# Kernel tuning notes

Measured on AMD Instinct MI355X. Metric: run time of the kernel, lower is better.

The kernel has to match this reference:

```python
import jax, jax.numpy as jnp
import numpy as np

B, S, D, H, MEL = 64, 512, 512, 8, 80
HD = D // H  # head dim


def _lstm_cell(x, h, c, w_ih, w_hh, b_ih, b_hh):
    # torch gate order: i, f, g, o
    gates = x @ w_ih.T + h @ w_hh.T + b_ih + b_hh
    i, f, g, o = jnp.split(gates, 4, axis=-1)
    c = jax.nn.sigmoid(f) * c + jax.nn.sigmoid(i) * jnp.tanh(g)
    h = jax.nn.sigmoid(o) * jnp.tanh(c)
    return h, c


def setup_inputs() -> dict:
    key = jax.random.key(0)
    ks = jax.random.split(key, 24)
    s = 0.05
    inp = {"encoder_output": jax.random.normal(ks[0], (B, S, D), jnp.float32)}
    # MultiheadAttention params (torch layout: in_proj [3D, D])
    inp["attn_in_w"] = jax.random.normal(ks[1], (3 * D, D), jnp.float32) * s
    inp["attn_in_b"] = jax.random.normal(ks[2], (3 * D,), jnp.float32) * s
    inp["attn_out_w"] = jax.random.normal(ks[3], (D, D), jnp.float32) * s
    inp["attn_out_b"] = jax.random.normal(ks[4], (D,), jnp.float32) * s
    # LSTM1 (2 layers)
    names = [("l1_w_ih0", (4 * D, D)), ("l1_w_hh0", (4 * D, D)), ("l1_b_ih0", (4 * D,)), ("l1_b_hh0", (4 * D,)),
             ("l1_w_ih1", (4 * D, D)), ("l1_w_hh1", (4 * D, D)), ("l1_b_ih1", (4 * D,)), ("l1_b_hh1", (4 * D,)),
             ("l2_w_ih", (4 * D, D)), ("l2_w_hh", (4 * D, D)), ("l2_b_ih", (4 * D,)), ("l2_b_hh", (4 * D,)),
             ("proj_w", (MEL, D)), ("proj_b", (MEL,))]
    for i, (n, shp) in enumerate(names):
        inp[n] = jax.random.normal(ks[5 + i], shp, jnp.float32) * s
    return inp


def reference(encoder_output, attn_in_w, attn_in_b, attn_out_w, attn_out_b,
              l1_w_ih0, l1_w_hh0, l1_b_ih0, l1_b_hh0,
              l1_w_ih1, l1_w_hh1, l1_b_ih1, l1_b_hh1,
              l2_w_ih, l2_w_hh, l2_b_ih, l2_b_hh, proj_w, proj_b):
    b, s, d = encoder_output.shape
    max_len = s * 5
    wq, wk, wv = jnp.split(attn_in_w, 3, axis=0)
    bq, bk, bv = jnp.split(attn_in_b, 3, axis=0)
    # Precompute K, V over encoder output: [B, S, H, HD]
    K = (encoder_output @ wk.T + bk).reshape(b, s, H, HD)
    V = (encoder_output @ wv.T + bv).reshape(b, s, H, HD)
    scale = 1.0 / np.sqrt(HD)

    def attend(x):  # x: [B, D] single-token query
        q = ((x @ wq.T + bq) * scale).reshape(b, H, HD)
        scores = jnp.einsum('bhd,bshd->bhs', q, K)
        w = jax.nn.softmax(scores, axis=-1)
        ctx = jnp.einsum('bhs,bshd->bhd', w, V).reshape(b, d)
        return ctx @ attn_out_w.T + attn_out_b

    zeros = jnp.zeros((b, d), encoder_output.dtype)
    carry0 = (zeros, zeros, zeros, zeros, zeros, zeros, zeros)

    def step(carry, _):
        h10, c10, h11, c11, h2, c2, dec_in = carry
        h10, c10 = _lstm_cell(dec_in, h10, c10, l1_w_ih0, l1_w_hh0, l1_b_ih0, l1_b_hh0)
        h11, c11 = _lstm_cell(h10, h11, c11, l1_w_ih1, l1_w_hh1, l1_b_ih1, l1_b_hh1)
        attn_out = attend(h11)
        h2, c2 = _lstm_cell(attn_out, h2, c2, l2_w_ih, l2_w_hh, l2_b_ih, l2_b_hh)
        out = h2 @ proj_w.T + proj_b  # [B, MEL]
        return (h10, c10, h11, c11, h2, c2, h2), out

    _, ys = jax.lax.scan(step, carry0, None, length=max_len)
    return jnp.transpose(ys, (1, 0, 2))  # [B, max_len, MEL]
```

## Files before the change

### kernel.cpp

```cpp
#include <hip/hip_runtime.h>
#include <hip/hip_bf16.h>
#include <hip/hip_fp8.h>

#define DEV_INLINE __device__ __forceinline__

typedef __attribute__((ext_vector_type(8))) short bf16x8;
typedef __attribute__((ext_vector_type(4))) float f32x4;
typedef unsigned long long ull;

constexpr int Bc = 64, Sc = 512, Dc = 512, Hc = 8, HDc = 64, MELc = 80, Tc = 2560;
constexpr int OUTSTRIDE = Tc * MELc;

constexpr size_t SZ_KP8 = 64ull * 8 * 512 * 64;
constexpr size_t SZ_VP8 = 64ull * 8 * 512 * 64;
constexpr size_t SZ_PL  = 128ull * 2048 * 16;
constexpr size_t OFF_KP8 = 0;
constexpr size_t OFF_VP8 = OFF_KP8 + SZ_KP8;
constexpr size_t OFF_PL0 = OFF_VP8 + SZ_VP8;
constexpr size_t OFF_PL1 = OFF_PL0 + SZ_PL;
constexpr size_t OFF_PL2 = OFF_PL1 + SZ_PL;
constexpr size_t OFF_PWQ = OFF_PL2 + SZ_PL;
constexpr size_t OFF_PP  = OFF_PWQ + 524288;
constexpr size_t OFF_BL0 = OFF_PP + 81920;
constexpr size_t OFF_BL1 = OFF_BL0 + 8192;
constexpr size_t OFF_BL2 = OFF_BL1 + 8192;
constexpr size_t OFF_B2E = OFF_BL2 + 8192;
constexpr size_t OFF_W2E = OFF_B2E + 8192;
constexpr size_t OFF_WOT = OFF_W2E + 2097152;
constexpr size_t OFF_ACT = OFF_WOT + 1048576;
constexpr size_t OFF_CTR = OFF_ACT + 524288;

constexpr unsigned LDS_WL0  = 0;
constexpr unsigned LDS_WL1  = 32768;
constexpr unsigned LDS_WL2  = 65536;
constexpr unsigned LDS_WPJ  = 98304;
constexpr unsigned LDS_PRED = 114688;
constexpr unsigned LDS_QLS  = 118784;
constexpr unsigned LDS_SCO  = 123136;
constexpr unsigned LDS_RED  = 127232;
constexpr unsigned LDS_CST  = 135424;
constexpr unsigned LDS_ST64 = 136960;
constexpr unsigned LDS_MISC = 137216;
constexpr unsigned DYN_LDS  = 137344;

DEV_INLINE unsigned* ctr_ptr(unsigned* base, int idx) { return base + idx * 32; }

DEV_INLINE float bf2f(short s) { return __uint_as_float(((unsigned)(unsigned short)s) << 16); }
DEV_INLINE short f2bf(float f) { union { __hip_bfloat16 h; short s; } u; u.h = __float2bfloat16(f); return u.s; }
DEV_INLINE float sig_f(float x) { return 1.0f / (1.0f + __expf(-x)); }
DEV_INLINE float tanh_f(float x) {
  float ax = fabsf(x);
  float e = __expf(fminf(2.0f * ax, 80.0f));
  float r = 1.0f - 2.0f / (e + 1.0f);
  return copysignf(r, x);
}
DEV_INLINE bf16x8 cvt8(const float* p) {
  bf16x8 r;
#pragma unroll
  for (int i = 0; i < 8; ++i) r[i] = f2bf(p[i]);
  return r;
}
DEV_INLINE float fp8tof(unsigned v) {
  __hip_fp8_e4m3 t; t.__x = (__hip_fp8_storage_t)v; return (float)t;
}

DEV_INLINE ull ld_dev_u64(const void* p) {
  return __hip_atomic_load((const ull*)p, __ATOMIC_RELAXED, __HIP_MEMORY_SCOPE_AGENT);
}
DEV_INLINE void st_dev_u64(void* p, ull v) {
  __hip_atomic_store((ull*)p, v, __ATOMIC_RELAXED, __HIP_MEMORY_SCOPE_AGENT);
}
DEV_INLINE bf16x8 ld_frag(const __hip_bfloat16* p) {
  union { bf16x8 v; ull u[2]; } r;
  r.u[0] = ld_dev_u64(p);
  r.u[1] = ld_dev_u64((const char*)p + 8);
  return r.v;
}

__global__ __launch_bounds__(256) void gemm_setup(const float* __restrict__ A,
                                                  const float* __restrict__ Bt,
                                                  const float* __restrict__ bias,
                                                  __hip_bfloat16* __restrict__ dst,
                                                  unsigned char* __restrict__ dst8,
                                                  int mode) {
  int tid = threadIdx.x, lane = tid & 63, wv = tid >> 6;
  int m0 = blockIdx.y * 64 + wv * 16;
  int nb = blockIdx.x * 64;
  int mrow = m0 + (lane & 15);
  int kb = (lane >> 4) * 8;
  f32x4 acc0 = {0,0,0,0}, acc1 = {0,0,0,0}, acc2 = {0,0,0,0}, acc3 = {0,0,0,0};
  const float* arow = A + (size_t)mrow * 512 + kb;
  const float* b0r = Bt + (size_t)(nb + 0 * 16 + (lane & 15)) * 512 + kb;
  const float* b1r = Bt + (size_t)(nb + 1 * 16 + (lane & 15)) * 512 + kb;
  const float* b2r = Bt + (size_t)(nb + 2 * 16 + (lane & 15)) * 512 + kb;
  const float* b3r = Bt + (size_t)(nb + 3 * 16 + (lane & 15)) * 512 + kb;
  for (int kk = 0; kk < 16; ++kk) {
    bf16x8 af = cvt8(arow + kk * 32);
    acc0 = __builtin_amdgcn_mfma_f32_16x16x32_bf16(af, cvt8(b0r + kk * 32), acc0, 0, 0, 0);
    acc1 = __builtin_amdgcn_mfma_f32_16x16x32_bf16(af, cvt8(b1r + kk * 32), acc1, 0, 0, 0);
    acc2 = __builtin_amdgcn_mfma_f32_16x16x32_bf16(af, cvt8(b2r + kk * 32), acc2, 0, 0, 0);
    acc3 = __builtin_amdgcn_mfma_f32_16x16x32_bf16(af, cvt8(b3r + kk * 32), acc3, 0, 0, 0);
  }
  int col16 = lane & 15, r0 = (lane >> 4) * 4;
  f32x4 accs[4] = {acc0, acc1, acc2, acc3};
#pragma unroll
  for (int nt = 0; nt < 4; ++nt) {
    int n = nb + nt * 16 + col16;
#pragma unroll
    for (int r = 0; r < 4; ++r) {
      int m = m0 + r0 + r;
      float v = accs[nt][r];
      if (mode == 2) {
        v += bias[n];
        int bb = m >> 9, s = m & 511, h = n >> 6, d = n & 63;
        __hip_fp8_e4m3 q(v);
        dst8[(((size_t)(bb * 8 + h) * 512 + s) * 64) + d] = (unsigned char)q.__x;
      } else {
        dst[(size_t)m * 512 + n] = __float2bfloat16(v);
      }
    }
  }
}

__global__ __launch_bounds__(256) void transpose512(const float* __restrict__ in, float* __restrict__ out) {
  __shared__ float tl[32][33];
  int x = threadIdx.x & 31, ty = threadIdx.x >> 5;
  int bx = blockIdx.x * 32, by = blockIdx.y * 32;
#pragma unroll
  for (int r = 0; r < 4; ++r) tl[ty + r * 8][x] = in[(size_t)(by + ty + r * 8) * 512 + bx + x];
  __syncthreads();
#pragma unroll
  for (int r = 0; r < 4; ++r) out[(size_t)(bx + ty + r * 8) * 512 + by + x] = tl[x][ty + r * 8];
}

__global__ __launch_bounds__(256) void b2eff_k(const float* __restrict__ w2ih, const float* __restrict__ bout,
                                               const float* __restrict__ bih, const float* __restrict__ bhh,
                                               float* __restrict__ dst) {
  int g = blockIdx.x * 256 + threadIdx.x;
  float acc = bih[g] + bhh[g];
  const float* row = w2ih + (size_t)g * 512;
  for (int k = 0; k < 512; ++k) acc += row[k] * bout[k];
  dst[g] = acc;
}

__global__ __launch_bounds__(256) void pack_lstm(const float* __restrict__ lo_f32,
                                                 const __hip_bfloat16* __restrict__ lo_bf16,
                                                 const float* __restrict__ hi_f32,
                                                 const float* __restrict__ b1, const float* __restrict__ b2,
                                                 const float* __restrict__ b_pre,
                                                 __hip_bfloat16* __restrict__ dst, float* __restrict__ bias_out,
                                                 int mode) {
  int u = blockIdx.x, tid = threadIdx.x;
  for (int rep = 0; rep < 8; ++rep) {
    int slot = rep * 256 + tid;
    int kk = slot >> 6, lane = slot & 63;
    int n16 = lane & 15, gate = n16 >> 2, jj = n16 & 3;
    int srow = gate * 512 + u * 4 + jj;
    int k = kk * 32 + (lane >> 4) * 8;
    __hip_bfloat16 tmp[8];
    if (k < 512) {
      if (mode == 0) {
#pragma unroll
        for (int i = 0; i < 8; ++i) tmp[i] = __float2bfloat16(lo_f32[(size_t)srow * 512 + k + i]);
      } else {
#pragma unroll
        for (int i = 0; i < 8; ++i) tmp[i] = lo_bf16[(size_t)srow * 512 + k + i];
      }
    } else {
#pragma unroll
      for (int i = 0; i < 8; ++i) tmp[i] = __float2bfloat16(hi_f32[(size_t)srow * 512 + (k - 512) + i]);
    }
    *(uint4*)(dst + ((size_t)u * 2048 + slot) * 8) = *(uint4*)tmp;
  }
  if (tid < 16) {
    int gate = tid >> 2, jj = tid & 3;
    int srow = gate * 512 + u * 4 + jj;
    bias_out[u * 16 + tid] = (mode == 0) ? (b1[srow] + b2[srow]) : b_pre[srow];
  }
}

__global__ __launch_bounds__(256) void pack_wq(const float* __restrict__ wq, __hip_bfloat16* __restrict__ dst) {
  int h = blockIdx.x, tid = threadIdx.x;
  for (int rep = 0; rep < 16; ++rep) {
    int slot = rep * 256 + tid;
    int nt = slot >> 10, kk = (slot >> 6) & 15, lane = slot & 63;
    int srow = h * 64 + nt * 16 + (lane & 15);
    int k = kk * 32 + (lane >> 4) * 8;
    __hip_bfloat16 tmp[8];
#pragma unroll
    for (int i = 0; i < 8; ++i) tmp[i] = __float2bfloat16(wq[(size_t)srow * 512 + k + i]);
    *(uint4*)(dst + ((size_t)h * 4096 + slot) * 8) = *(uint4*)tmp;
  }
}

__global__ __launch_bounds__(256) void pack_proj(const float* __restrict__ pw, __hip_bfloat16* __restrict__ dst) {
  int u5 = blockIdx.x, tid = threadIdx.x;
  for (int rep = 0; rep < 4; ++rep) {
    int slot = rep * 256 + tid;
    int kk = slot >> 6, lane = slot & 63;
    int srow = u5 * 16 + (lane & 15);
    int k = kk * 32 + (lane >> 4) * 8;
    __hip_bfloat16 tmp[8];
#pragma unroll
    for (int i = 0; i < 8; ++i) tmp[i] = __float2bfloat16(pw[(size_t)srow * 512 + k + i]);
    *(uint4*)(dst + ((size_t)u5 * 1024 + slot) * 8) = *(uint4*)tmp;
  }
}

struct DecParams {
  const float* attn_in_b;
  const float* proj_b;
  const uint4* packL0; const uint4* packL1; const uint4* packL2;
  const float* biasL0; const float* biasL1; const float* biasL2;
  const uint4* packWq; const uint4* packP;
  const unsigned char* Kp8; const unsigned char* Vp8;
  __hip_bfloat16* h10b; __hip_bfloat16* h11b; __hip_bfloat16* h2b; __hip_bfloat16* ctxb;
  ull* actbase;
  unsigned* ctrs;
  float* out;
};

constexpr ull WD_TICKS = 200000000ull;

DEV_INLINE void publish_ctr(unsigned* c, int tid) {
  __builtin_amdgcn_s_waitcnt(0);
  __syncthreads();
  if (tid == 0)
    (void)__hip_atomic_fetch_add(c, 1u, __ATOMIC_RELAXED, __HIP_MEMORY_SCOPE_AGENT);
}

DEV_INLINE bool wait_ctr(const unsigned* c, unsigned target, int tid,
                         ull t0, int* bail) {
  if (tid == 0) {
    while (__hip_atomic_load(c, __ATOMIC_RELAXED, __HIP_MEMORY_SCOPE_AGENT) < target) {
      if (__builtin_amdgcn_s_memrealtime() - t0 > WD_TICKS) { *bail = 1; break; }
      __builtin_amdgcn_s_sleep(1);
    }
  }
  __syncthreads();
  return !*bail;
}

DEV_INLINE void prefetch_hi(bf16x8* pf, const __hip_bfloat16* hi, int g, int lane, int wv) {
  if (wv >= 2) {
    const __hip_bfloat16* p = hi + (size_t)(g * 32 + (wv & 1) * 16 + (lane & 15)) * 512 + (lane >> 4) * 8;
#pragma unroll
    for (int kk = 0; kk < 16; ++kk) pf[kk] = ld_frag(p + kk * 32);
  }
}

DEV_INLINE void lstm_stage(int tid, int g, int wgl,
                           const uint4* wlds, const float* bias,
                           const __hip_bfloat16* lo, const bf16x8* pf,
                           float* cstate, __hip_bfloat16* hc,
                           float* pred, ull* st64) {
  const int lane = tid & 63, wv = tid >> 6, mt = wv & 1, kh = wv >> 1;
  f32x4 acc = {0,0,0,0};
  if (kh == 0) {
    const __hip_bfloat16* pA = lo + (size_t)(g * 32 + mt * 16 + (lane & 15)) * 512 + (lane >> 4) * 8;
#pragma unroll
    for (int kk = 0; kk < 16; ++kk) {
      bf16x8 a = ld_frag(pA + kk * 32);
      bf16x8 b = *(const bf16x8*)(wlds + kk * 64 + lane);
      acc = __builtin_amdgcn_mfma_f32_16x16x32_bf16(a, b, acc, 0, 0, 0);
    }
  } else {
#pragma unroll
    for (int kk = 0; kk < 16; ++kk) {
      bf16x8 b = *(const bf16x8*)(wlds + (16 + kk) * 64 + lane);
      acc = __builtin_amdgcn_mfma_f32_16x16x32_bf16(pf[kk], b, acc, 0, 0, 0);
    }
  }
#pragma unroll
  for (int r = 0; r < 4; ++r) pred[wv * 256 + lane * 4 + r] = acc[r];
  __syncthreads();
  if (tid < 128) {
    int bl = tid >> 2, j = tid & 3;
    int mt2 = bl >> 4, qd = (bl & 15) >> 2, reg = bl & 3;
    const float* p0 = pred + mt2 * 256;
    const float* p1 = pred + (2 + mt2) * 256;
    int l0 = qd * 16;
    float gi = p0[(l0 + j) * 4 + reg]      + p1[(l0 + j) * 4 + reg]      + bias[j];
    float gf = p0[(l0 + 4 + j) * 4 + reg]  + p1[(l0 + 4 + j) * 4 + reg]  + bias[4 + j];
    float gg = p0[(l0 + 8 + j) * 4 + reg]  + p1[(l0 + 8 + j) * 4 + reg]  + bias[8 + j];
    float go = p0[(l0 + 12 + j) * 4 + reg] + p1[(l0 + 12 + j) * 4 + reg] + bias[12 + j];
    float c = cstate[tid & 127];
    c = sig_f(gf) * c + sig_f(gi) * tanh_f(gg);
    float h = sig_f(go) * tanh_f(c);
    cstate[tid & 127] = c;
    ((unsigned short*)st64)[tid] = (unsigned short)f2bf(h);
  }
  __syncthreads();
  if (tid < 32)
    st_dev_u64(hc + (size_t)(g * 32 + tid) * 512 + wgl * 4, st64[tid]);
}

DEV_INLINE void proj_stage(int tid, int g, int n5, const uint4* wPJ, const float* proj_b,
                           const __hip_bfloat16* h2in, float* outp, float* pred) {
  const int lane = tid & 63, wv = tid >> 6, mt = wv & 1, kh = wv >> 1;
  f32x4 acc = {0,0,0,0};
  const __hip_bfloat16* pA = h2in + (size_t)(g * 32 + mt * 16 + (lane & 15)) * 512 + kh * 256 + (lane >> 4) * 8;
#pragma unroll
  for (int kk = 0; kk < 8; ++kk) {
    bf16x8 a = ld_frag(pA + kk * 32);
    bf16x8 b = *(const bf16x8*)(wPJ + (kh * 8 + kk) * 64 + lane);
    acc = __builtin_amdgcn_mfma_f32_16x16x32_bf16(a, b, acc, 0, 0, 0);
  }
#pragma unroll
  for (int r = 0; r < 4; ++r) pred[wv * 256 + lane * 4 + r] = acc[r];
  __syncthreads();
#pragma unroll
  for (int half = 0; half < 2; ++half) {
    int gx = half * 256 + tid;
    int row = gx >> 4, col = gx & 15;
    int mt2 = row >> 4, qd = (row & 15) >> 2, reg = row & 3, ln = qd * 16 + col;
    float v = pred[mt2 * 256 + ln * 4 + reg] + pred[(2 + mt2) * 256 + ln * 4 + reg] + proj_b[n5 * 16 + col];
    outp[(size_t)(g * 32 + row) * OUTSTRIDE + n5 * 16 + col] = v;
  }
  __syncthreads();
}

__global__ __launch_bounds__(256, 1) void decoder_main(DecParams P) {
  extern __shared__ char smem[];
  uint4* wL0  = (uint4*)(smem + LDS_WL0);
  uint4* wL1  = (uint4*)(smem + LDS_WL1);
  uint4* wL2  = (uint4*)(smem + LDS_WL2);
  uint4* wPJ  = (uint4*)(smem + LDS_WPJ);
  float* pred = (float*)(smem + LDS_PRED);
  float* qls  = (float*)(smem + LDS_QLS);
  float* sco  = (float*)(smem + LDS_SCO);
  float* red  = (float*)(smem + LDS_RED);
  float* cst  = (float*)(smem + LDS_CST);
  ull*   st64 = (ull*)(smem + LDS_ST64);
  float* smx  = (float*)(smem + LDS_MISC);
  float* ssum = smx + 4;
  float* sinv = ssum + 4;
  int*   sbail = (int*)(sinv + 2);

  const int wg = blockIdx.x, tid = threadIdx.x;
  const int lane = tid & 63, wv = tid >> 6;
  const int g = wg >> 7;
  const int wgl = wg & 127;
  const int hh = wgl >> 4;
  const int b0g = (wgl & 15) * 2;
  const int bblk = b0g & ~15;

  const ull t0 = __builtin_amdgcn_s_memrealtime();
  unsigned* cInit = ctr_ptr(P.ctrs, 0);
  unsigned* cA = ctr_ptr(P.ctrs, 1 + g * 4 + 0);
  unsigned* cB = ctr_ptr(P.ctrs, 1 + g * 4 + 1);
  unsigned* cC = ctr_ptr(P.ctrs, 1 + g * 4 + 2);
  unsigned* cD = ctr_ptr(P.ctrs, 1 + g * 4 + 3);

  {
    const uint4* s0 = P.packL0 + (size_t)wgl * 2048;
    const uint4* s1 = P.packL1 + (size_t)wgl * 2048;
    const uint4* s2 = P.packL2 + (size_t)wgl * 2048;
    for (int i = tid; i < 2048; i += 256) { wL0[i] = s0[i]; wL1[i] = s1[i]; wL2[i] = s2[i]; }
    if (wgl < 5) { const uint4* sp = P.packP + (size_t)wgl * 1024; for (int i = tid; i < 1024; i += 256) wPJ[i] = sp[i]; }
  }
  if (tid == 0) *sbail = 0;
  if (tid < 128) { cst[tid] = 0.0f; cst[128 + tid] = 0.0f; cst[256 + tid] = 0.0f; }
  st_dev_u64(P.actbase + (size_t)wg * 256 + tid, 0ull);
  __syncthreads();
  publish_ctr(cInit, tid);
  if (!wait_ctr(cInit, 256u, tid, t0, sbail)) goto bail;

  for (int t = 0; t < Tc; ++t) {
    const int cur = t & 1, pv = cur ^ 1;
    const unsigned stepN = 128u * (unsigned)(t + 1);
    __hip_bfloat16* h10c = P.h10b + cur * 32768; __hip_bfloat16* h10p = P.h10b + pv * 32768;
    __hip_bfloat16* h11c = P.h11b + cur * 32768; __hip_bfloat16* h11p = P.h11b + pv * 32768;
    __hip_bfloat16* h2c  = P.h2b  + cur * 32768; __hip_bfloat16* h2p  = P.h2b  + pv * 32768;
    __hip_bfloat16* ctxc = P.ctxb + cur * 32768;

    {
      bf16x8 pf[16];
      prefetch_hi(pf, h10p, g, lane, wv);
      if (t > 0 && !wait_ctr(cD, stepN - 128u, tid, t0, sbail)) goto bail;
      lstm_stage(tid, g, wgl, wL0, P.biasL0 + wgl * 16, h2p, pf, cst, h10c, pred, st64);
      publish_ctr(cA, tid);
    }
    if (wgl < 5 && t > 0)
      proj_stage(tid, g, wgl, wPJ, P.proj_b, h2p, P.out + (size_t)(t - 1) * MELc, pred);

    {
      bf16x8 pf[16];
      prefetch_hi(pf, h11p, g, lane, wv);
      if (!wait_ctr(cA, stepN, tid, t0, sbail)) goto bail;
      lstm_stage(tid, g, wgl, wL1, P.biasL1 + wgl * 16, h10c, pf, cst + 128, h11c, pred, st64);
      publish_ctr(cB, tid);
    }

    if (!wait_ctr(cB, stepN, tid, t0, sbail)) goto bail;
    {
      int mrow = g * 32 + bblk + (lane & 15);
      const __hip_bfloat16* pA = h11c + (size_t)mrow * 512 + (lane >> 4) * 8;
      const uint4* pB = P.packWq + (size_t)hh * 4096 + wv * 1024;
      f32x4 acc = {0,0,0,0};
#pragma unroll
      for (int kk = 0; kk < 16; ++kk) {
        bf16x8 a = ld_frag(pA + kk * 32);
        bf16x8 b = *(const bf16x8*)(pB + kk * 64 + lane);
        acc = __builtin_amdgcn_mfma_f32_16x16x32_bf16(a, b, acc, 0, 0, 0);
      }
      int col = lane & 15, row0 = (lane >> 4) << 2;
      int dg = wv * 16 + col;
      float bq = P.attn_in_b[hh * 64 + dg];
#pragma unroll
      for (int r = 0; r < 4; ++r) qls[(row0 + r) * 68 + dg] = (acc[r] + bq) * 0.125f;
    }
    __syncthreads();
    {
      int p = tid >> 7, si = tid & 127;
      int bg = g * 32 + b0g + p;
      const float* qv = qls + ((b0g & 15) + p) * 68;
      const ull* Kb = (const ull*)(P.Kp8 + (size_t)(bg * 8 + hh) * 512 * 64);
#pragma unroll
      for (int ss = 0; ss < 4; ++ss) {
        int s = si * 4 + ss;
        const ull* kr = Kb + (size_t)s * 8;
        float acc = 0.0f;
#pragma unroll
        for (int i = 0; i < 8; ++i) {
          ull kv = kr[i];
#pragma unroll
          for (int jj = 0; jj < 8; ++jj)
            acc += qv[i * 8 + jj] * fp8tof((unsigned)(kv >> (8 * jj)) & 0xFFu);
        }
        sco[p * 512 + s] = acc;
      }
    }
    __syncthreads();
    {
      int p = wv >> 1, half = wv & 1;
      int idx = tid & 127;
      float mx = -1e30f;
#pragma unroll
      for (int ss = 0; ss < 4; ++ss) mx = fmaxf(mx, sco[p * 512 + idx * 4 + ss]);
#pragma unroll
      for (int off = 32; off; off >>= 1) mx = fmaxf(mx, __shfl_xor(mx, off));
      if (lane == 0) smx[p * 2 + half] = mx;
      __syncthreads();
      float m = fmaxf(smx[p * 2], smx[p * 2 + 1]);
      float sum = 0.0f;
#pragma unroll
      for (int ss = 0; ss < 4; ++ss) {
        int ix = p * 512 + idx * 4 + ss;
        float e = __expf(sco[ix] - m);
        sco[ix] = e; sum += e;
      }
#pragma unroll
      for (int off = 32; off; off >>= 1) sum += __shfl_xor(sum, off);
      if (lane == 0) ssum[p * 2 + half] = sum;
      __syncthreads();
      if (tid < 2) sinv[tid] = 1.0f / (ssum[tid * 2] + ssum[tid * 2 + 1]);
    }
    __syncthreads();
    {
      int p = wv >> 1, half = wv & 1;
      int bg = g * 32 + b0g + p;
      int sg = lane >> 3, dj = lane & 7;
      const unsigned char* Vb = P.Vp8 + (size_t)(bg * 8 + hh) * 512 * 64;
      float a8[8] = {0,0,0,0,0,0,0,0};
      for (int it = 0; it < 32; ++it) {
        int s = half * 256 + it * 8 + sg;
        float w = sco[p * 512 + s];
        ull v = *(const ull*)(Vb + (size_t)s * 64 + dj * 8);
#pragma unroll
        for (int e = 0; e < 8; ++e) a8[e] += w * fp8tof((unsigned)(v >> (8 * e)) & 0xFFu);
      }
      float* rp = red + ((p * 16 + half * 8 + sg) * 64) + dj * 8;
#pragma unroll
      for (int e = 0; e < 8; ++e) rp[e] = a8[e];
    }
    __syncthreads();
    if (tid < 128) {
      int p = tid >> 6, d = tid & 63;
      float sacc = 0.0f;
#pragma unroll
      for (int k = 0; k < 16; ++k) sacc += red[(p * 16 + k) * 64 + d];
      sacc *= sinv[p];
      ((unsigned short*)st64)[tid] = (unsigned short)f2bf(sacc);
    }
    __syncthreads();
    if (tid < 32) {
      int p = tid >> 4, q = tid & 15;
      st_dev_u64(ctxc + (size_t)(g * 32 + b0g + p) * 512 + hh * 64 + q * 4, st64[p * 16 + q]);
    }
    publish_ctr(cC, tid);

    {
      bf16x8 pf[16];
      prefetch_hi(pf, h2p, g, lane, wv);
      if (!wait_ctr(cC, stepN, tid, t0, sbail)) goto bail;
      lstm_stage(tid, g, wgl, wL2, P.biasL2 + wgl * 16, ctxc, pf, cst + 256, h2c, pred, st64);
      publish_ctr(cD, tid);
    }
  }

  if (wgl < 5) {
    if (wait_ctr(cD, 128u * (unsigned)Tc, tid, t0, sbail))
      proj_stage(tid, g, wgl, wPJ, P.proj_b, P.h2b + ((Tc - 1) & 1) * 32768,
                 P.out + (size_t)(Tc - 1) * MELc, pred);
  }
  return;

bail:
  if (tid == 0)
    for (int i = 0; i < 9; ++i)
      (void)__hip_atomic_fetch_add(ctr_ptr(P.ctrs, i), 0x01000000u,
                                   __ATOMIC_RELAXED, __HIP_MEMORY_SCOPE_AGENT);
}

extern "C" void kernel_launch(void* const* d_in, const int* in_sizes, int n_in,
                              void* d_out, int out_size, void* d_ws, size_t ws_size,
                              hipStream_t stream) {
  const float* enc        = (const float*)d_in[0];
  const float* attn_in_w  = (const float*)d_in[1];
  const float* attn_in_b  = (const float*)d_in[2];
  const float* attn_out_w = (const float*)d_in[3];
  const float* attn_out_b = (const float*)d_in[4];
  const float* w_ih0 = (const float*)d_in[5];
  const float* w_hh0 = (const float*)d_in[6];
  const float* b_ih0 = (const float*)d_in[7];
  const float* b_hh0 = (const float*)d_in[8];
  const float* w_ih1 = (const float*)d_in[9];
  const float* w_hh1 = (const float*)d_in[10];
  const float* b_ih1 = (const float*)d_in[11];
  const float* b_hh1 = (const float*)d_in[12];
  const float* w_ih2 = (const float*)d_in[13];
  const float* w_hh2 = (const float*)d_in[14];
  const float* b_ih2 = (const float*)d_in[15];
  const float* b_hh2 = (const float*)d_in[16];
  const float* proj_w = (const float*)d_in[17];
  const float* proj_b = (const float*)d_in[18];

  char* ws = (char*)d_ws;
  unsigned char*  Kp8 = (unsigned char*)(ws + OFF_KP8);
  unsigned char*  Vp8 = (unsigned char*)(ws + OFF_VP8);
  __hip_bfloat16* pl0 = (__hip_bfloat16*)(ws + OFF_PL0);
  __hip_bfloat16* pl1 = (__hip_bfloat16*)(ws + OFF_PL1);
  __hip_bfloat16* pl2 = (__hip_bfloat16*)(ws + OFF_PL2);
  __hip_bfloat16* pwq = (__hip_bfloat16*)(ws + OFF_PWQ);
  __hip_bfloat16* pp  = (__hip_bfloat16*)(ws + OFF_PP);
  float* bl0 = (float*)(ws + OFF_BL0);
  float* bl1 = (float*)(ws + OFF_BL1);
  float* bl2 = (float*)(ws + OFF_BL2);
  float* b2e = (float*)(ws + OFF_B2E);
  __hip_bfloat16* w2e = (__hip_bfloat16*)(ws + OFF_W2E);
  float* wot = (float*)(ws + OFF_WOT);
  char* act  = ws + OFF_ACT;
  unsigned* ctrs = (unsigned*)(ws + OFF_CTR);

  hipMemsetAsync(ctrs, 0, 4096, stream);

  gemm_setup<<<dim3(8, 512), 256, 0, stream>>>(enc, attn_in_w + 512 * 512, attn_in_b + 512, nullptr, Kp8, 2);
  gemm_setup<<<dim3(8, 512), 256, 0, stream>>>(enc, attn_in_w + 1024 * 512, attn_in_b + 1024, nullptr, Vp8, 2);
  transpose512<<<dim3(16, 16), 256, 0, stream>>>(attn_out_w, wot);
  gemm_setup<<<dim3(8, 32), 256, 0, stream>>>(w_ih2, wot, nullptr, w2e, nullptr, 1);
  b2eff_k<<<8, 256, 0, stream>>>(w_ih2, attn_out_b, b_ih2, b_hh2, b2e);
  pack_lstm<<<128, 256, 0, stream>>>(w_ih0, nullptr, w_hh0, b_ih0, b_hh0, nullptr, pl0, bl0, 0);
  pack_lstm<<<128, 256, 0, stream>>>(w_ih1, nullptr, w_hh1, b_ih1, b_hh1, nullptr, pl1, bl1, 0);
  pack_lstm<<<128, 256, 0, stream>>>(nullptr, w2e, w_hh2, nullptr, nullptr, b2e, pl2, bl2, 1);
  pack_wq<<<8, 256, 0, stream>>>(attn_in_w, pwq);
  pack_proj<<<5, 256, 0, stream>>>(proj_w, pp);

  DecParams p;
  p.attn_in_b = attn_in_b;
  p.proj_b = proj_b;
  p.packL0 = (const uint4*)pl0; p.packL1 = (const uint4*)pl1; p.packL2 = (const uint4*)pl2;
  p.biasL0 = bl0; p.biasL1 = bl1; p.biasL2 = bl2;
  p.packWq = (const uint4*)pwq; p.packP = (const uint4*)pp;
  p.Kp8 = Kp8; p.Vp8 = Vp8;
  p.h10b = (__hip_bfloat16*)(act + 0);
  p.h11b = (__hip_bfloat16*)(act + 131072);
  p.h2b  = (__hip_bfloat16*)(act + 262144);
  p.ctxb = (__hip_bfloat16*)(act + 393216);
  p.actbase = (ull*)act;
  p.ctrs = ctrs;
  p.out = (float*)d_out;

  (void)hipFuncSetAttribute((const void*)decoder_main,
                            hipFuncAttributeMaxDynamicSharedMemorySize, DYN_LDS);
  decoder_main<<<dim3(256), dim3(256), DYN_LDS, stream>>>(p);
}
```

Baseline: 115.8 ms.

## Replace atomic counters with per-workgroup flag bytes and spread projection across workgroups

```diff
diff --git a/kernel.cpp b/kernel.cpp
--- a/kernel.cpp
+++ b/kernel.cpp
@@ -20,30 +20,26 @@
 constexpr size_t OFF_PL1 = OFF_PL0 + SZ_PL;
 constexpr size_t OFF_PL2 = OFF_PL1 + SZ_PL;
 constexpr size_t OFF_PWQ = OFF_PL2 + SZ_PL;
-constexpr size_t OFF_PP  = OFF_PWQ + 524288;
-constexpr size_t OFF_BL0 = OFF_PP + 81920;
+constexpr size_t OFF_BL0 = OFF_PWQ + 524288;
 constexpr size_t OFF_BL1 = OFF_BL0 + 8192;
 constexpr size_t OFF_BL2 = OFF_BL1 + 8192;
 constexpr size_t OFF_B2E = OFF_BL2 + 8192;
 constexpr size_t OFF_W2E = OFF_B2E + 8192;
 constexpr size_t OFF_WOT = OFF_W2E + 2097152;
 constexpr size_t OFF_ACT = OFF_WOT + 1048576;
-constexpr size_t OFF_CTR = OFF_ACT + 524288;
+constexpr size_t OFF_FLG = OFF_ACT + 524288;
 
 constexpr unsigned LDS_WL0  = 0;
 constexpr unsigned LDS_WL1  = 32768;
 constexpr unsigned LDS_WL2  = 65536;
-constexpr unsigned LDS_WPJ  = 98304;
-constexpr unsigned LDS_PRED = 114688;
-constexpr unsigned LDS_QLS  = 118784;
-constexpr unsigned LDS_SCO  = 123136;
-constexpr unsigned LDS_RED  = 127232;
-constexpr unsigned LDS_CST  = 135424;
-constexpr unsigned LDS_ST64 = 136960;
-constexpr unsigned LDS_MISC = 137216;
-constexpr unsigned DYN_LDS  = 137344;
-
-DEV_INLINE unsigned* ctr_ptr(unsigned* base, int idx) { return base + idx * 32; }
+constexpr unsigned LDS_PRED = 98304;
+constexpr unsigned LDS_QLS  = 102400;
+constexpr unsigned LDS_SCO  = 106752;
+constexpr unsigned LDS_RED  = 110848;
+constexpr unsigned LDS_CST  = 119040;
+constexpr unsigned LDS_ST64 = 120576;
+constexpr unsigned LDS_MISC = 120832;
+constexpr unsigned DYN_LDS  = 120896;
 
 DEV_INLINE float bf2f(short s) { return __uint_as_float(((unsigned)(unsigned short)s) << 16); }
 DEV_INLINE short f2bf(float f) { union { __hip_bfloat16 h; short s; } u; u.h = __float2bfloat16(f); return u.s; }
@@ -64,17 +60,11 @@
   __hip_fp8_e4m3 t; t.__x = (__hip_fp8_storage_t)v; return (float)t;
 }
 
-DEV_INLINE ull ld_dev_u64(const void* p) {
-  return __hip_atomic_load((const ull*)p, __ATOMIC_RELAXED, __HIP_MEMORY_SCOPE_AGENT);
-}
 DEV_INLINE void st_dev_u64(void* p, ull v) {
   __hip_atomic_store((ull*)p, v, __ATOMIC_RELAXED, __HIP_MEMORY_SCOPE_AGENT);
 }
-DEV_INLINE bf16x8 ld_frag(const __hip_bfloat16* p) {
-  union { bf16x8 v; ull u[2]; } r;
-  r.u[0] = ld_dev_u64(p);
-  r.u[1] = ld_dev_u64((const char*)p + 8);
-  return r.v;
+DEV_INLINE void st_dev_f32(float* p, float v) {
+  __hip_atomic_store(p, v, __ATOMIC_RELAXED, __HIP_MEMORY_SCOPE_AGENT);
 }
 
 __global__ __launch_bounds__(256) void gemm_setup(const float* __restrict__ A,
@@ -193,59 +183,62 @@
   }
 }
 
-__global__ __launch_bounds__(256) void pack_proj(const float* __restrict__ pw, __hip_bfloat16* __restrict__ dst) {
-  int u5 = blockIdx.x, tid = threadIdx.x;
-  for (int rep = 0; rep < 4; ++rep) {
-    int slot = rep * 256 + tid;
-    int kk = slot >> 6, lane = slot & 63;
-    int srow = u5 * 16 + (lane & 15);
-    int k = kk * 32 + (lane >> 4) * 8;
-    __hip_bfloat16 tmp[8];
-#pragma unroll
-    for (int i = 0; i < 8; ++i) tmp[i] = __float2bfloat16(pw[(size_t)srow * 512 + k + i]);
-    *(uint4*)(dst + ((size_t)u5 * 1024 + slot) * 8) = *(uint4*)tmp;
-  }
-}
-
 struct DecParams {
   const float* attn_in_b;
   const float* proj_b;
+  const float* projW;
   const uint4* packL0; const uint4* packL1; const uint4* packL2;
   const float* biasL0; const float* biasL1; const float* biasL2;
-  const uint4* packWq; const uint4* packP;
+  const uint4* packWq;
   const unsigned char* Kp8; const unsigned char* Vp8;
   __hip_bfloat16* h10b; __hip_bfloat16* h11b; __hip_bfloat16* h2b; __hip_bfloat16* ctxb;
   ull* actbase;
-  unsigned* ctrs;
+  unsigned char* flags;
   float* out;
 };
 
 constexpr ull WD_TICKS = 200000000ull;
 
-DEV_INLINE void publish_ctr(unsigned* c, int tid) {
+DEV_INLINE void publish_flag(unsigned char* flags, int wg, unsigned char v, int tid) {
   __builtin_amdgcn_s_waitcnt(0);
   __syncthreads();
   if (tid == 0)
-    (void)__hip_atomic_fetch_add(c, 1u, __ATOMIC_RELAXED, __HIP_MEMORY_SCOPE_AGENT);
-}
-
-DEV_INLINE bool wait_ctr(const unsigned* c, unsigned target, int tid,
-                         ull t0, int* bail) {
-  if (tid == 0) {
-    while (__hip_atomic_load(c, __ATOMIC_RELAXED, __HIP_MEMORY_SCOPE_AGENT) < target) {
-      if (__builtin_amdgcn_s_memrealtime() - t0 > WD_TICKS) { *bail = 1; break; }
+    __hip_atomic_store(&flags[wg], v, __ATOMIC_RELAXED, __HIP_MEMORY_SCOPE_AGENT);
+}
+
+DEV_INLINE bool wait_flags(const unsigned char* flags, int base, int nflags,
+                           unsigned char v, int tid, ull t0, int* sbail) {
+  const ull pat = 0x0101010101010101ull * (ull)v;
+  const int nq = nflags >> 3;
+  if (tid < 64) {
+    const ull* p = (const ull*)(flags + base) + tid;
+    const ull* dp = (const ull*)(flags + 256);
+    for (;;) {
+      bool ok = true, dead = false;
+      if (tid < nq)
+        ok = (__hip_atomic_load(p, __ATOMIC_RELAXED, __HIP_MEMORY_SCOPE_AGENT) == pat);
+      if (tid == nq)
+        dead = (__hip_atomic_load(dp, __ATOMIC_RELAXED, __HIP_MEMORY_SCOPE_AGENT) != 0);
+      if (__any(dead ? 1 : 0) ||
+          (__builtin_amdgcn_s_memrealtime() - t0 > WD_TICKS)) {
+        if (tid == 0) *sbail = 1;
+        break;
+      }
+      if (__all(ok ? 1 : 0)) break;
       __builtin_amdgcn_s_sleep(1);
     }
   }
   __syncthreads();
-  return !*bail;
+  if (*sbail) return false;
+  __builtin_amdgcn_fence(__ATOMIC_ACQUIRE, "agent");
+  return true;
 }
 
 DEV_INLINE void prefetch_hi(bf16x8* pf, const __hip_bfloat16* hi, int g, int lane, int wv) {
   if (wv >= 2) {
     const __hip_bfloat16* p = hi + (size_t)(g * 32 + (wv & 1) * 16 + (lane & 15)) * 512 + (lane >> 4) * 8;
 #pragma unroll
-    for (int kk = 0; kk < 16; ++kk) pf[kk] = ld_frag(p + kk * 32);
+    for (int kk = 0; kk < 16; ++kk) pf[kk] = *(const bf16x8*)(p + kk * 32);
   }
 }
 
@@ -260,7 +253,7 @@
     const __hip_bfloat16* pA = lo + (size_t)(g * 32 + mt * 16 + (lane & 15)) * 512 + (lane >> 4) * 8;
 #pragma unroll
     for (int kk = 0; kk < 16; ++kk) {
-      bf16x8 a = ld_frag(pA + kk * 32);
+      bf16x8 a = *(const bf16x8*)(pA + kk * 32);
       bf16x8 b = *(const bf16x8*)(wlds + kk * 64 + lane);
       acc = __builtin_amdgcn_mfma_f32_16x16x32_bf16(a, b, acc, 0, 0, 0);
     }
@@ -295,29 +288,27 @@
     st_dev_u64(hc + (size_t)(g * 32 + tid) * 512 + wgl * 4, st64[tid]);
 }
 
-DEV_INLINE void proj_stage(int tid, int g, int n5, const uint4* wPJ, const float* proj_b,
-                           const __hip_bfloat16* h2in, float* outp, float* pred) {
-  const int lane = tid & 63, wv = tid >> 6, mt = wv & 1, kh = wv >> 1;
-  f32x4 acc = {0,0,0,0};
-  const __hip_bfloat16* pA = h2in + (size_t)(g * 32 + mt * 16 + (lane & 15)) * 512 + kh * 256 + (lane >> 4) * 8;
-#pragma unroll
-  for (int kk = 0; kk < 8; ++kk) {
-    bf16x8 a = ld_frag(pA + kk * 32);
-    bf16x8 b = *(const bf16x8*)(wPJ + (kh * 8 + kk) * 64 + lane);
-    acc = __builtin_amdgcn_mfma_f32_16x16x32_bf16(a, b, acc, 0, 0, 0);
-  }
-#pragma unroll
-  for (int r = 0; r < 4; ++r) pred[wv * 256 + lane * 4 + r] = acc[r];
-  __syncthreads();
-#pragma unroll
-  for (int half = 0; half < 2; ++half) {
-    int gx = half * 256 + tid;
-    int row = gx >> 4, col = gx & 15;
-    int mt2 = row >> 4, qd = (row & 15) >> 2, reg = row & 3, ln = qd * 16 + col;
-    float v = pred[mt2 * 256 + ln * 4 + reg] + pred[(2 + mt2) * 256 + ln * 4 + reg] + proj_b[n5 * 16 + col];
-    outp[(size_t)(g * 32 + row) * OUTSTRIDE + n5 * 16 + col] = v;
-  }
-  __syncthreads();
+DEV_INLINE void proj_spread(int tid, int g, int wgl, const float* projW,
+                            const float* proj_b, const __hip_bfloat16* h2in,
+                            float* outp) {
+  int i = tid >> 3, k8 = tid & 7;
+  if (i < 20) {
+    int o = wgl * 20 + i;
+    int row = o / 80, col = o - row * 80;
+    const __hip_bfloat16* hr = h2in + (size_t)(g * 32 + row) * 512 + k8 * 64;
+    const float* wr = projW + (size_t)col * 512 + k8 * 64;
+    float acc = 0.0f;
+#pragma unroll
+    for (int k = 0; k < 64; k += 8) {
+      bf16x8 hv = *(const bf16x8*)(hr + k);
+#pragma unroll
+      for (int e = 0; e < 8; ++e) acc += bf2f(hv[e]) * wr[k + e];
+    }
+#pragma unroll
+    for (int off = 4; off; off >>= 1) acc += __shfl_down(acc, off);
+    if (k8 == 0)
+      st_dev_f32(&outp[(size_t)(g * 32 + row) * OUTSTRIDE + col], acc + proj_b[col]);
+  }
 }
 
 __global__ __launch_bounds__(256, 1) void decoder_main(DecParams P) {
@@ -325,7 +316,6 @@
   uint4* wL0  = (uint4*)(smem + LDS_WL0);
   uint4* wL1  = (uint4*)(smem + LDS_WL1);
   uint4* wL2  = (uint4*)(smem + LDS_WL2);
-  uint4* wPJ  = (uint4*)(smem + LDS_WPJ);
   float* pred = (float*)(smem + LDS_PRED);
   float* qls  = (float*)(smem + LDS_QLS);
   float* sco  = (float*)(smem + LDS_SCO);
@@ -341,34 +331,34 @@
   const int lane = tid & 63, wv = tid >> 6;
   const int g = wg >> 7;
   const int wgl = wg & 127;
+  const int fbase = g * 128;
   const int hh = wgl >> 4;
   const int b0g = (wgl & 15) * 2;
   const int bblk = b0g & ~15;
 
   const ull t0 = __builtin_amdgcn_s_memrealtime();
-  unsigned* cInit = ctr_ptr(P.ctrs, 0);
-  unsigned* cA = ctr_ptr(P.ctrs, 1 + g * 4 + 0);
-  unsigned* cB = ctr_ptr(P.ctrs, 1 + g * 4 + 1);
-  unsigned* cC = ctr_ptr(P.ctrs, 1 + g * 4 + 2);
-  unsigned* cD = ctr_ptr(P.ctrs, 1 + g * 4 + 3);
+  unsigned char* flags = P.flags;
 
   {
     const uint4* s0 = P.packL0 + (size_t)wgl * 2048;
     const uint4* s1 = P.packL1 + (size_t)wgl * 2048;
     const uint4* s2 = P.packL2 + (size_t)wgl * 2048;
     for (int i = tid; i < 2048; i += 256) { wL0[i] = s0[i]; wL1[i] = s1[i]; wL2[i] = s2[i]; }
-    if (wgl < 5) { const uint4* sp = P.packP + (size_t)wgl * 1024; for (int i = tid; i < 1024; i += 256) wPJ[i] = sp[i]; }
   }
   if (tid == 0) *sbail = 0;
   if (tid < 128) { cst[tid] = 0.0f; cst[128 + tid] = 0.0f; cst[256 + tid] = 0.0f; }
   st_dev_u64(P.actbase + (size_t)wg * 256 + tid, 0ull);
   __syncthreads();
-  publish_ctr(cInit, tid);
-  if (!wait_ctr(cInit, 256u, tid, t0, sbail)) goto bail;
+  publish_flag(flags, wg, 1u, tid);
+  if (!wait_flags(flags, 0, 256, 1u, tid, t0, sbail)) goto bail;
 
   for (int t = 0; t < Tc; ++t) {
     const int cur = t & 1, pv = cur ^ 1;
-    const unsigned stepN = 128u * (unsigned)(t + 1);
+    const unsigned char wA = (unsigned char)(4 * t + 1);
+    const unsigned char vA = (unsigned char)(4 * t + 2);
+    const unsigned char vB = (unsigned char)(4 * t + 3);
+    const unsigned char vC = (unsigned char)(4 * t + 4);
+    const unsigned char vD = (unsigned char)(4 * t + 5);
     __hip_bfloat16* h10c = P.h10b + cur * 32768; __hip_bfloat16* h10p = P.h10b + pv * 32768;
     __hip_bfloat16* h11c = P.h11b + cur * 32768; __hip_bfloat16* h11p = P.h11b + pv * 32768;
     __hip_bfloat16* h2c  = P.h2b  + cur * 32768; __hip_bfloat16* h2p  = P.h2b  + pv * 32768;
@@ -377,22 +367,22 @@
     {
       bf16x8 pf[16];
       prefetch_hi(pf, h10p, g, lane, wv);
-      if (t > 0 && !wait_ctr(cD, stepN - 128u, tid, t0, sbail)) goto bail;
+      if (t > 0 && !wait_flags(flags, fbase, 128, wA, tid, t0, sbail)) goto bail;
       lstm_stage(tid, g, wgl, wL0, P.biasL0 + wgl * 16, h2p, pf, cst, h10c, pred, st64);
-      publish_ctr(cA, tid);
-    }
-    if (wgl < 5 && t > 0)
-      proj_stage(tid, g, wgl, wPJ, P.proj_b, h2p, P.out + (size_t)(t - 1) * MELc, pred);
+      publish_flag(flags, wg, vA, tid);
+    }
+    if (t > 0)
+      proj_spread(tid, g, wgl, P.projW, P.proj_b, h2p, P.out + (size_t)(t - 1) * MELc);
 
     {
       bf16x8 pf[16];
       prefetch_hi(pf, h11p, g, lane, wv);
-      if (!wait_ctr(cA, stepN, tid, t0, sbail)) goto bail;
+      if (!wait_flags(flags, fbase, 128, vA, tid, t0, sbail)) goto bail;
       lstm_stage(tid, g, wgl, wL1, P.biasL1 + wgl * 16, h10c, pf, cst + 128, h11c, pred, st64);
-      publish_ctr(cB, tid);
-    }
-
-    if (!wait_ctr(cB, stepN, tid, t0, sbail)) goto bail;
+      publish_flag(flags, wg, vB, tid);
+    }
+
+    if (!wait_flags(flags, fbase, 128, vB, tid, t0, sbail)) goto bail;
     {
       int mrow = g * 32 + bblk + (lane & 15);
       const __hip_bfloat16* pA = h11c + (size_t)mrow * 512 + (lane >> 4) * 8;
@@ -400,7 +390,7 @@
       f32x4 acc = {0,0,0,0};
 #pragma unroll
       for (int kk = 0; kk < 16; ++kk) {
-        bf16x8 a = ld_frag(pA + kk * 32);
+        bf16x8 a = *(const bf16x8*)(pA + kk * 32);
         bf16x8 b = *(const bf16x8*)(pB + kk * 64 + lane);
         acc = __builtin_amdgcn_mfma_f32_16x16x32_bf16(a, b, acc, 0, 0, 0);
       }
@@ -488,29 +478,24 @@
       int p = tid >> 4, q = tid & 15;
       st_dev_u64(ctxc + (size_t)(g * 32 + b0g + p) * 512 + hh * 64 + q * 4, st64[p * 16 + q]);
     }
-    publish_ctr(cC, tid);
+    publish_flag(flags, wg, vC, tid);
 
     {
       bf16x8 pf[16];
       prefetch_hi(pf, h2p, g, lane, wv);
-      if (!wait_ctr(cC, stepN, tid, t0, sbail)) goto bail;
+      if (!wait_flags(flags, fbase, 128, vC, tid, t0, sbail)) goto bail;
       lstm_stage(tid, g, wgl, wL2, P.biasL2 + wgl * 16, ctxc, pf, cst + 256, h2c, pred, st64);
-      publish_ctr(cD, tid);
-    }
-  }
-
-  if (wgl < 5) {
-    if (wait_ctr(cD, 128u * (unsigned)Tc, tid, t0, sbail))
-      proj_stage(tid, g, wgl, wPJ, P.proj_b, P.h2b + ((Tc - 1) & 1) * 32768,
-                 P.out + (size_t)(Tc - 1) * MELc, pred);
-  }
+      publish_flag(flags, wg, vD, tid);
+    }
+  }
+
+  if (wait_flags(flags, fbase, 128, (unsigned char)(4 * Tc + 1), tid, t0, sbail))
+    proj_spread(tid, g, wgl, P.projW, P.proj_b,
+                P.h2b + ((Tc - 1) & 1) * 32768, P.out + (size_t)(Tc - 1) * MELc);
   return;
 
 bail:
-  if (tid == 0)
-    for (int i = 0; i < 9; ++i)
-      (void)__hip_atomic_fetch_add(ctr_ptr(P.ctrs, i), 0x01000000u,
-                                   __ATOMIC_RELAXED, __HIP_MEMORY_SCOPE_AGENT);
+  if (tid == 0) st_dev_u64(flags + 256, ~0ull);
 }
 
 extern "C" void kernel_launch(void* const* d_in, const int* in_sizes, int n_in,
@@ -543,7 +528,6 @@
   __hip_bfloat16* pl1 = (__hip_bfloat16*)(ws + OFF_PL1);
   __hip_bfloat16* pl2 = (__hip_bfloat16*)(ws + OFF_PL2);
   __hip_bfloat16* pwq = (__hip_bfloat16*)(ws + OFF_PWQ);
-  __hip_bfloat16* pp  = (__hip_bfloat16*)(ws + OFF_PP);
   float* bl0 = (float*)(ws + OFF_BL0);
   float* bl1 = (float*)(ws + OFF_BL1);
   float* bl2 = (float*)(ws + OFF_BL2);
@@ -551,9 +535,9 @@
   __hip_bfloat16* w2e = (__hip_bfloat16*)(ws + OFF_W2E);
   float* wot = (float*)(ws + OFF_WOT);
   char* act  = ws + OFF_ACT;
-  unsigned* ctrs = (unsigned*)(ws + OFF_CTR);
-
-  hipMemsetAsync(ctrs, 0, 4096, stream);
+  unsigned char* flags = (unsigned char*)(ws + OFF_FLG);
+
+  hipMemsetAsync(flags, 0, 4096, stream);
 
   gemm_setup<<<dim3(8, 512), 256, 0, stream>>>(enc, attn_in_w + 512 * 512, attn_in_b + 512, nullptr, Kp8, 2);
   gemm_setup<<<dim3(8, 512), 256, 0, stream>>>(enc, attn_in_w + 1024 * 512, attn_in_b + 1024, nullptr, Vp8, 2);
@@ -564,21 +548,21 @@
   pack_lstm<<<128, 256, 0, stream>>>(w_ih1, nullptr, w_hh1, b_ih1, b_hh1, nullptr, pl1, bl1, 0);
   pack_lstm<<<128, 256, 0, stream>>>(nullptr, w2e, w_hh2, nullptr, nullptr, b2e, pl2, bl2, 1);
   pack_wq<<<8, 256, 0, stream>>>(attn_in_w, pwq);
-  pack_proj<<<5, 256, 0, stream>>>(proj_w, pp);
 
   DecParams p;
   p.attn_in_b = attn_in_b;
   p.proj_b = proj_b;
+  p.projW = proj_w;
   p.packL0 = (const uint4*)pl0; p.packL1 = (const uint4*)pl1; p.packL2 = (const uint4*)pl2;
   p.biasL0 = bl0; p.biasL1 = bl1; p.biasL2 = bl2;
-  p.packWq = (const uint4*)pwq; p.packP = (const uint4*)pp;
+  p.packWq = (const uint4*)pwq;
   p.Kp8 = Kp8; p.Vp8 = Vp8;
   p.h10b = (__hip_bfloat16*)(act + 0);
   p.h11b = (__hip_bfloat16*)(act + 131072);
   p.h2b  = (__hip_bfloat16*)(act + 262144);
   p.ctxb = (__hip_bfloat16*)(act + 393216);
   p.actbase = (ull*)act;
-  p.ctrs = ctrs;
+  p.flags = flags;
   p.out = (float*)d_out;
 
   (void)hipFuncSetAttribute((const void*)decoder_main,
```

After: 181.2 ms. 1.56x slower.
